# Optimization experiments

Measured on AMD Instinct MI355X. Metric: run time of the kernel, lower is better.

The kernel has to match this reference:

```python
import jax, jax.numpy as jnp
import numpy as np
from jax.scipy.linalg import solve_triangular

B, H, W, C, K = 8, 256, 256, 8, 16  # batch, height, width, channel_num, class_num


def setup_inputs() -> dict:
    key = jax.random.key(0)
    k1, k2, k3 = jax.random.split(key, 3)
    x = jax.random.normal(k1, (B, H, W, C), dtype=jnp.float32)
    # scale_tril weights: small random lower-ish matrix + identity on diag for
    # numerically sane Gaussian pdfs (layer init is 'uniform' near zero; we
    # shift the diagonal so probs are finite but the math is identical).
    scale = (0.1 * jax.random.normal(k2, (K, 1, C, C), dtype=jnp.float32)
             + jnp.eye(C, dtype=jnp.float32)[None, None])
    mean = 0.05 * jax.random.normal(k3, (K, 1, C), dtype=jnp.float32)
    return {"x": x, "scale": scale, "mean": mean}


def _forward(x, scale, mean):
    b = x.shape[0]
    hw = H * W
    xf = x.reshape(b, hw, C)                     # [B, HW, C]
    L = scale[:, 0]                               # [K, C, C] (lower tri used)
    mu = mean[:, 0]                               # [K, C]

    # MultivariateNormalTriL.prob: q = ||L^{-1}(x-mu)||^2, computed once per
    # (class, pixel) without tiling L/mu across pixels.
    diff = xf[None] - mu[:, None, None, :]        # [K, B, HW, C]
    d = diff.reshape(K, b * hw, C).transpose(0, 2, 1)  # [K, C, B*HW]
    y = solve_triangular(L, d, lower=True)        # [K, C, B*HW]
    quad = jnp.sum(y * y, axis=1)                 # [K, B*HW]
    log_det = jnp.sum(jnp.log(jnp.abs(jnp.diagonal(L, axis1=1, axis2=2))), axis=1)  # [K]
    log2pi = jnp.log(jnp.asarray(2.0 * np.pi, dtype=x.dtype))
    logp = -0.5 * quad - log_det[:, None] - 0.5 * C * log2pi
    gauss = jnp.exp(logp).reshape(K, b, hw)       # [K, B, HW]

    # output[i*C + j] = gauss[i] * x[..., j]  -> [K, C, B, HW]
    x_ch = xf.transpose(2, 0, 1)                  # [C, B, HW]
    outs = gauss[:, None, :, :] * x_ch[None]      # [K, C, B, HW]
    # Faithful to tf.reshape([K*C, B, HW] -> [B, H, W, K*C]) raw row-major reshape
    out = outs.reshape(K * C, b, hw).reshape(b, H, W, K * C)
    return jnp.concatenate([x.reshape(b, H, W, C), out], axis=3)


def reference(x, scale, mean):
    return _forward(x, scale, mean)
```

## Files before the change

### kernel.cpp

```cpp
#include <hip/hip_runtime.h>

#define S_TOTAL 524288u
#define NEG4LOG2PI (-7.3515082656373808f)

typedef float f32x4 __attribute__((ext_vector_type(4)));

__global__ void prep_kernel(const float* __restrict__ scale,
                            float* __restrict__ minv,
                            float* __restrict__ base) {
    int k = threadIdx.x;
    if (k >= 16) return;
    float L[8][8], M[8][8];
    const float* Ls = scale + k * 64;
    for (int i = 0; i < 8; i++)
        for (int j = 0; j < 8; j++) { L[i][j] = Ls[i * 8 + j]; M[i][j] = 0.f; }
    for (int j = 0; j < 8; j++) {
        M[j][j] = 1.0f / L[j][j];
        for (int i = j + 1; i < 8; i++) {
            float s = 0.f;
            for (int m = j; m < i; m++) s += L[i][m] * M[m][j];
            M[i][j] = -s / L[i][i];
        }
    }
    float logdet = 0.f;
    for (int i = 0; i < 8; i++) logdet += logf(fabsf(L[i][i]));
    for (int i = 0; i < 8; i++)
        for (int j = 0; j < 8; j++) minv[k * 64 + i * 8 + j] = M[i][j];
    base[k] = -logdet + NEG4LOG2PI;
}

template <bool INLINE_PREP>
__global__ __launch_bounds__(256) void fused_kernel(
    const float* __restrict__ x,
    const float* __restrict__ minv,
    const float* __restrict__ base,
    const float* __restrict__ mean,
    const float* __restrict__ scale,
    float* __restrict__ out)
{
    __shared__ float sM[1024];
    __shared__ float sMu[128];
    __shared__ float sB[16];
    __shared__ float sXrT[8][128];
    __shared__ float sGT[16][128];
    __shared__ float sXq[128][8];

    const unsigned t  = threadIdx.x;
    const unsigned r0 = blockIdx.x;

    if (INLINE_PREP) {
        if (t < 16u) {
            float L[8][8], M[8][8];
            const float* Ls = scale + t * 64u;
            for (int i = 0; i < 8; i++)
                for (int j = 0; j < 8; j++) { L[i][j] = Ls[i * 8 + j]; M[i][j] = 0.f; }
            for (int j = 0; j < 8; j++) {
                M[j][j] = 1.0f / L[j][j];
                for (int i = j + 1; i < 8; i++) {
                    float s = 0.f;
                    for (int m = j; m < i; m++) s += L[i][m] * M[m][j];
                    M[i][j] = -s / L[i][i];
                }
            }
            float logdet = 0.f;
            for (int i = 0; i < 8; i++) logdet += logf(fabsf(L[i][i]));
            for (int i = 0; i < 8; i++)
                for (int j = 0; j < 8; j++) sM[t * 64u + i * 8 + j] = M[i][j];
            sB[t] = -logdet + NEG4LOG2PI;
        }
    } else {
        for (unsigned i = t; i < 1024u; i += 256u) sM[i] = minv[i];
        if (t < 16u) sB[t] = base[t];
    }
    if (t < 128u) sMu[t] = mean[t];

    {
        f32x4 v = ((const f32x4*)x)[r0 * 256u + t];
        unsigned p = t >> 1, h = (t & 1u) * 4u;
        sXrT[h + 0][p] = v.x; sXrT[h + 1][p] = v.y;
        sXrT[h + 2][p] = v.z; sXrT[h + 3][p] = v.w;
    }
    {
        unsigned kc = t >> 1, h = t & 1u;
        f32x4 v = ((const f32x4*)x)[(kc * 4096u + r0) * 2u + h];
        unsigned b = h * 4u;
        sXq[kc][b + 0] = v.x; sXq[kc][b + 1] = v.y;
        sXq[kc][b + 2] = v.z; sXq[kc][b + 3] = v.w;
    }
    __syncthreads();

    {
        unsigned j  = t & 127u;
        unsigned k0 = (t >> 7) * 8u;
        float xv[8];
        #pragma unroll
        for (int c = 0; c < 8; c++) xv[c] = sXrT[c][j];
        #pragma unroll
        for (unsigned kk = 0; kk < 8u; kk++) {
            unsigned k = k0 + kk;
            const float* M  = &sM[k * 64u];
            const float* mu = &sMu[k * 8u];
            float d[8];
            #pragma unroll
            for (int c = 0; c < 8; c++) d[c] = xv[c] - mu[c];
            float quad = 0.f;
            #pragma unroll
            for (int i = 0; i < 8; i++) {
                float y = 0.f;
                #pragma unroll
                for (int jj = 0; jj <= i; jj++) y = fmaf(M[i * 8 + jj], d[jj], y);
                quad = fmaf(y, y, quad);
            }
            sGT[k][j] = __expf(fmaf(-0.5f, quad, sB[k]));
        }
    }
    __syncthreads();

    for (unsigned i = t; i < 4352u; i += 256u) {
        unsigned kc = i / 34u;
        unsigned f4 = i - kc * 34u;
        f32x4 v;
        if (f4 < 2u) {
            v = *(const f32x4*)&sXq[kc][f4 * 4u];
        } else {
            unsigned j0 = f4 * 4u - 8u;
            unsigned k  = kc >> 3, c = kc & 7u;
            f32x4 g  = *(const f32x4*)&sGT[k][j0];
            f32x4 xc = *(const f32x4*)&sXrT[c][j0];
            v = g * xc;
        }
        float* dst = out + (kc * 4096u + r0) * 136u + f4 * 4u;
        __builtin_nontemporal_store(v, (f32x4*)dst);
    }
}

extern "C" void kernel_launch(void* const* d_in, const int* in_sizes, int n_in,
                              void* d_out, int out_size, void* d_ws, size_t ws_size,
                              hipStream_t stream) {
    const float* x     = (const float*)d_in[0];
    const float* scale = (const float*)d_in[1];
    const float* mean  = (const float*)d_in[2];
    float* out = (float*)d_out;

    const size_t NEED = (1024 + 16) * sizeof(float);
    if (ws_size >= NEED) {
        float* minv = (float*)d_ws;
        float* base = minv + 1024;
        prep_kernel<<<1, 64, 0, stream>>>(scale, minv, base);
        fused_kernel<false><<<4096, 256, 0, stream>>>(x, minv, base, mean, scale, out);
    } else {
        fused_kernel<true><<<4096, 256, 0, stream>>>(x, nullptr, nullptr, mean, scale, out);
    }
}
```

Measured before the change: 345.2 us.

## Split fused kernel work by class and pixel chunk per block

Each block now handles one class k and a 2048-pixel chunk in two 1024-pixel groups, instead of one output row across all 16 classes. Each block loads only its own class's inverse matrix, mean and base, and keeps the pixel channels in one transposed shared tile that is reused for the Gaussian evaluation and the output product. The passthrough x copy is spread across class blocks. This cuts per-block shared state and changes the store access pattern, but adds an extra barrier per group and rereads x once for each of the 16 classes.

```diff
diff --git a/kernel.cpp b/kernel.cpp
--- a/kernel.cpp
+++ b/kernel.cpp
@@ -38,20 +38,21 @@
     const float* __restrict__ scale,
     float* __restrict__ out)
 {
-    __shared__ float sM[1024];
-    __shared__ float sMu[128];
-    __shared__ float sB[16];
-    __shared__ float sXrT[8][128];
-    __shared__ float sGT[16][128];
-    __shared__ float sXq[128][8];
+    __shared__ float sXT[8][1024];
+    __shared__ float sG[1024];
+    __shared__ float sM[64];
+    __shared__ float sMu[8];
+    __shared__ float sB_;
 
-    const unsigned t  = threadIdx.x;
-    const unsigned r0 = blockIdx.x;
+    const unsigned t     = threadIdx.x;
+    const unsigned bid   = blockIdx.x;
+    const unsigned chunk = bid >> 4;
+    const unsigned k     = bid & 15u;
 
     if (INLINE_PREP) {
-        if (t < 16u) {
+        if (t == 0) {
             float L[8][8], M[8][8];
-            const float* Ls = scale + t * 64u;
+            const float* Ls = scale + k * 64u;
             for (int i = 0; i < 8; i++)
                 for (int j = 0; j < 8; j++) { L[i][j] = Ls[i * 8 + j]; M[i][j] = 0.f; }
             for (int j = 0; j < 8; j++) {
@@ -65,72 +66,68 @@
             float logdet = 0.f;
             for (int i = 0; i < 8; i++) logdet += logf(fabsf(L[i][i]));
             for (int i = 0; i < 8; i++)
-                for (int j = 0; j < 8; j++) sM[t * 64u + i * 8 + j] = M[i][j];
-            sB[t] = -logdet + NEG4LOG2PI;
+                for (int j = 0; j < 8; j++) sM[i * 8 + j] = M[i][j];
+            sB_ = -logdet + NEG4LOG2PI;
         }
     } else {
-        for (unsigned i = t; i < 1024u; i += 256u) sM[i] = minv[i];
-        if (t < 16u) sB[t] = base[t];
+        if (t < 64u) sM[t] = minv[k * 64u + t];
+        if (t == 64u) sB_ = base[k];
     }
-    if (t < 128u) sMu[t] = mean[t];
+    if (t < 8u) sMu[t] = mean[k * 8u + t];
 
-    {
-        f32x4 v = ((const f32x4*)x)[r0 * 256u + t];
-        unsigned p = t >> 1, h = (t & 1u) * 4u;
-        sXrT[h + 0][p] = v.x; sXrT[h + 1][p] = v.y;
-        sXrT[h + 2][p] = v.z; sXrT[h + 3][p] = v.w;
-    }
-    {
-        unsigned kc = t >> 1, h = t & 1u;
-        f32x4 v = ((const f32x4*)x)[(kc * 4096u + r0) * 2u + h];
-        unsigned b = h * 4u;
-        sXq[kc][b + 0] = v.x; sXq[kc][b + 1] = v.y;
-        sXq[kc][b + 2] = v.z; sXq[kc][b + 3] = v.w;
-    }
-    __syncthreads();
+    for (unsigned g = 0; g < 2u; ++g) {
+        const unsigned px_base = chunk * 2048u + g * 1024u;
 
-    {
-        unsigned j  = t & 127u;
-        unsigned k0 = (t >> 7) * 8u;
-        float xv[8];
         #pragma unroll
-        for (int c = 0; c < 8; c++) xv[c] = sXrT[c][j];
+        for (unsigned pass = 0; pass < 8u; ++pass) {
+            unsigned idx = pass * 256u + t;
+            f32x4 v = ((const f32x4*)x)[px_base * 2u + idx];
+            unsigned p = idx >> 1, h = (idx & 1u) * 4u;
+            sXT[h + 0][p] = v.x; sXT[h + 1][p] = v.y;
+            sXT[h + 2][p] = v.z; sXT[h + 3][p] = v.w;
+        }
+        __syncthreads();
+
         #pragma unroll
-        for (unsigned kk = 0; kk < 8u; kk++) {
-            unsigned k = k0 + kk;
-            const float* M  = &sM[k * 64u];
-            const float* mu = &sMu[k * 8u];
+        for (unsigned pp = 0; pp < 4u; ++pp) {
+            unsigned p = pp * 256u + t;
             float d[8];
             #pragma unroll
-            for (int c = 0; c < 8; c++) d[c] = xv[c] - mu[c];
+            for (int c = 0; c < 8; c++) d[c] = sXT[c][p] - sMu[c];
             float quad = 0.f;
             #pragma unroll
             for (int i = 0; i < 8; i++) {
                 float y = 0.f;
                 #pragma unroll
-                for (int jj = 0; jj <= i; jj++) y = fmaf(M[i * 8 + jj], d[jj], y);
+                for (int j = 0; j <= i; j++) y = fmaf(sM[i * 8 + j], d[j], y);
                 quad = fmaf(y, y, quad);
             }
-            sGT[k][j] = __expf(fmaf(-0.5f, quad, sB[k]));
+            sG[p] = __expf(fmaf(-0.5f, quad, sB_));
         }
-    }
-    __syncthreads();
+        __syncthreads();
 
-    for (unsigned i = t; i < 4352u; i += 256u) {
-        unsigned kc = i / 34u;
-        unsigned f4 = i - kc * 34u;
-        f32x4 v;
-        if (f4 < 2u) {
-            v = *(const f32x4*)&sXq[kc][f4 * 4u];
-        } else {
-            unsigned j0 = f4 * 4u - 8u;
-            unsigned k  = kc >> 3, c = kc & 7u;
-            f32x4 g  = *(const f32x4*)&sGT[k][j0];
-            f32x4 xc = *(const f32x4*)&sXrT[c][j0];
-            v = g * xc;
+        #pragma unroll
+        for (unsigned pass = 0; pass < 8u; ++pass) {
+            unsigned i  = pass * 256u + t;
+            unsigned c  = i >> 8;
+            unsigned rr = (i >> 5) & 7u;
+            unsigned f2 = i & 31u;
+            unsigned p  = rr * 128u + f2 * 4u;
+            f32x4 gv = *(const f32x4*)&sG[p];
+            f32x4 xc = *(const f32x4*)&sXT[c][p];
+            f32x4 v  = gv * xc;
+            unsigned q = (k * 8u + c) * 4096u + chunk * 16u + g * 8u + rr;
+            __builtin_nontemporal_store(v, (f32x4*)(out + q * 136u + 8u + f2 * 4u));
         }
-        float* dst = out + (kc * 4096u + r0) * 136u + f4 * 4u;
-        __builtin_nontemporal_store(v, (f32x4*)dst);
+        if (t < 128u) {
+            unsigned c  = t >> 4;
+            unsigned rr = (t >> 1) & 7u;
+            unsigned h  = t & 1u;
+            unsigned q  = (k * 8u + c) * 4096u + chunk * 16u + g * 8u + rr;
+            f32x4 v = ((const f32x4*)x)[q * 2u + h];
+            __builtin_nontemporal_store(v, (f32x4*)(out + q * 136u + h * 4u));
+        }
+        __syncthreads();
     }
 }
 
```

After: 360.3 us. +4.4%, slower.

## Split fused kernel into gauss/transpose pass and streaming output sweep

Applied to the files above, without the earlier changes.

Replaces the single fused kernel with two kernels when workspace allows. The first computes all 16 Gaussian densities per pixel and writes them, along with a channel-transposed copy of x, to workspace. The second streams the output rows contiguously, each block handling one (k,c) slab. The goal is to make the output writes fully sequential per block and to avoid the scattered x gathers of the fused version. The cost is an extra round trip of about 100MB through global memory.

```diff
diff --git a/kernel.cpp b/kernel.cpp
--- a/kernel.cpp
+++ b/kernel.cpp
@@ -29,11 +29,85 @@
     base[k] = -logdet + NEG4LOG2PI;
 }
 
-template <bool INLINE_PREP>
-__global__ __launch_bounds__(256) void fused_kernel(
+__global__ __launch_bounds__(256) void gauss_xt_kernel(
     const float* __restrict__ x,
     const float* __restrict__ minv,
     const float* __restrict__ base,
+    const float* __restrict__ mean,
+    float* __restrict__ gauss,
+    float* __restrict__ xt)
+{
+    __shared__ float sM[1024];
+    __shared__ float sMu[128];
+    __shared__ float sB[16];
+    for (int i = threadIdx.x; i < 1024; i += 256) sM[i] = minv[i];
+    if (threadIdx.x < 128) sMu[threadIdx.x] = mean[threadIdx.x];
+    if (threadIdx.x < 16)  sB[threadIdx.x] = base[threadIdx.x];
+    __syncthreads();
+
+    unsigned s = blockIdx.x * 256u + threadIdx.x;
+    f32x4 a = ((const f32x4*)x)[s * 2u];
+    f32x4 b = ((const f32x4*)x)[s * 2u + 1u];
+    float xv[8] = {a.x, a.y, a.z, a.w, b.x, b.y, b.z, b.w};
+
+    #pragma unroll
+    for (int c = 0; c < 8; c++) xt[c * S_TOTAL + s] = xv[c];
+
+    #pragma unroll
+    for (int k = 0; k < 16; k++) {
+        const float* M  = &sM[k * 64];
+        const float* mu = &sMu[k * 8];
+        float d[8];
+        #pragma unroll
+        for (int c = 0; c < 8; c++) d[c] = xv[c] - mu[c];
+        float quad = 0.f;
+        #pragma unroll
+        for (int i = 0; i < 8; i++) {
+            float y = 0.f;
+            #pragma unroll
+            for (int j = 0; j <= i; j++) y = fmaf(M[i * 8 + j], d[j], y);
+            quad = fmaf(y, y, quad);
+        }
+        gauss[k * S_TOTAL + s] = __expf(fmaf(-0.5f, quad, sB[k]));
+    }
+}
+
+__global__ __launch_bounds__(256) void out_sweep_kernel(
+    const float* __restrict__ x,
+    const float* __restrict__ gauss,
+    const float* __restrict__ xt,
+    float* __restrict__ out)
+{
+    const unsigned t   = threadIdx.x;
+    const unsigned b   = blockIdx.x;
+    const unsigned kc  = b >> 5;
+    const unsigned k   = kc >> 3, c = kc & 7u;
+    const unsigned rb  = (b & 31u) * 128u;
+    const unsigned q0  = kc * 4096u + rb;
+
+    const f32x4* __restrict__ gk = (const f32x4*)(gauss + (size_t)k * S_TOTAL) + rb * 32u;
+    const f32x4* __restrict__ xc = (const f32x4*)(xt    + (size_t)c * S_TOTAL) + rb * 32u;
+    const f32x4* __restrict__ xh = (const f32x4*)(x + (size_t)q0 * 8u);
+    f32x4* __restrict__ o = (f32x4*)(out + (size_t)q0 * 136u);
+
+    #pragma unroll
+    for (unsigned pass = 0; pass < 17u; ++pass) {
+        unsigned i   = pass * 256u + t;
+        unsigned r   = i / 34u;
+        unsigned ch4 = i - r * 34u;
+        f32x4 v;
+        if (ch4 < 2u) {
+            v = xh[r * 2u + ch4];
+        } else {
+            unsigned idx = r * 32u + (ch4 - 2u);
+            v = gk[idx] * xc[idx];
+        }
+        __builtin_nontemporal_store(v, o + i);
+    }
+}
+
+__global__ __launch_bounds__(256) void fused_kernel(
+    const float* __restrict__ x,
     const float* __restrict__ mean,
     const float* __restrict__ scale,
     float* __restrict__ out)
@@ -48,29 +122,24 @@
     const unsigned t  = threadIdx.x;
     const unsigned r0 = blockIdx.x;
 
-    if (INLINE_PREP) {
-        if (t < 16u) {
-            float L[8][8], M[8][8];
-            const float* Ls = scale + t * 64u;
-            for (int i = 0; i < 8; i++)
-                for (int j = 0; j < 8; j++) { L[i][j] = Ls[i * 8 + j]; M[i][j] = 0.f; }
-            for (int j = 0; j < 8; j++) {
-                M[j][j] = 1.0f / L[j][j];
-                for (int i = j + 1; i < 8; i++) {
-                    float s = 0.f;
-                    for (int m = j; m < i; m++) s += L[i][m] * M[m][j];
-                    M[i][j] = -s / L[i][i];
-                }
+    if (t < 16u) {
+        float L[8][8], M[8][8];
+        const float* Ls = scale + t * 64u;
+        for (int i = 0; i < 8; i++)
+            for (int j = 0; j < 8; j++) { L[i][j] = Ls[i * 8 + j]; M[i][j] = 0.f; }
+        for (int j = 0; j < 8; j++) {
+            M[j][j] = 1.0f / L[j][j];
+            for (int i = j + 1; i < 8; i++) {
+                float s = 0.f;
+                for (int m = j; m < i; m++) s += L[i][m] * M[m][j];
+                M[i][j] = -s / L[i][i];
             }
-            float logdet = 0.f;
-            for (int i = 0; i < 8; i++) logdet += logf(fabsf(L[i][i]));
-            for (int i = 0; i < 8; i++)
-                for (int j = 0; j < 8; j++) sM[t * 64u + i * 8 + j] = M[i][j];
-            sB[t] = -logdet + NEG4LOG2PI;
-        }
-    } else {
-        for (unsigned i = t; i < 1024u; i += 256u) sM[i] = minv[i];
-        if (t < 16u) sB[t] = base[t];
+        }
+        float logdet = 0.f;
+        for (int i = 0; i < 8; i++) logdet += logf(fabsf(L[i][i]));
+        for (int i = 0; i < 8; i++)
+            for (int j = 0; j < 8; j++) sM[t * 64u + i * 8 + j] = M[i][j];
+        sB[t] = -logdet + NEG4LOG2PI;
     }
     if (t < 128u) sMu[t] = mean[t];
 
@@ -83,9 +152,9 @@
     {
         unsigned kc = t >> 1, h = t & 1u;
         f32x4 v = ((const f32x4*)x)[(kc * 4096u + r0) * 2u + h];
-        unsigned b = h * 4u;
-        sXq[kc][b + 0] = v.x; sXq[kc][b + 1] = v.y;
-        sXq[kc][b + 2] = v.z; sXq[kc][b + 3] = v.w;
+        unsigned bofs = h * 4u;
+        sXq[kc][bofs + 0] = v.x; sXq[kc][bofs + 1] = v.y;
+        sXq[kc][bofs + 2] = v.z; sXq[kc][bofs + 3] = v.w;
     }
     __syncthreads();
 
@@ -126,8 +195,8 @@
             unsigned j0 = f4 * 4u - 8u;
             unsigned k  = kc >> 3, c = kc & 7u;
             f32x4 g  = *(const f32x4*)&sGT[k][j0];
-            f32x4 xc = *(const f32x4*)&sXrT[c][j0];
-            v = g * xc;
+            f32x4 xcv = *(const f32x4*)&sXrT[c][j0];
+            v = g * xcv;
         }
         float* dst = out + (kc * 4096u + r0) * 136u + f4 * 4u;
         __builtin_nontemporal_store(v, (f32x4*)dst);
@@ -142,13 +211,19 @@
     const float* mean  = (const float*)d_in[2];
     float* out = (float*)d_out;
 
-    const size_t NEED = (1024 + 16) * sizeof(float);
+    const size_t GAUSS_BYTES = (size_t)16 * S_TOTAL * 4;
+    const size_t XT_BYTES    = (size_t)8  * S_TOTAL * 4;
+    const size_t NEED = GAUSS_BYTES + XT_BYTES + (1024 + 16) * sizeof(float);
+
     if (ws_size >= NEED) {
-        float* minv = (float*)d_ws;
-        float* base = minv + 1024;
+        float* gauss = (float*)d_ws;
+        float* xt    = (float*)((char*)d_ws + GAUSS_BYTES);
+        float* minv  = (float*)((char*)d_ws + GAUSS_BYTES + XT_BYTES);
+        float* base  = minv + 1024;
         prep_kernel<<<1, 64, 0, stream>>>(scale, minv, base);
-        fused_kernel<false><<<4096, 256, 0, stream>>>(x, minv, base, mean, scale, out);
+        gauss_xt_kernel<<<S_TOTAL / 256, 256, 0, stream>>>(x, minv, base, mean, gauss, xt);
+        out_sweep_kernel<<<4096, 256, 0, stream>>>(x, gauss, xt, out);
     } else {
-        fused_kernel<true><<<4096, 256, 0, stream>>>(x, nullptr, nullptr, mean, scale, out);
-    }
-}
+        fused_kernel<<<4096, 256, 0, stream>>>(x, mean, scale, out);
+    }
+}
```

Result: faster. 314.6 us (-8.9%).
